# Performance work log

Hardware: AMD Instinct MI355X
Metric: run time of the kernel (lower is better)

The kernel has to match this reference:

```python
import jax, jax.numpy as jnp
import numpy as np

B, S, IN_F, OUT_F, GROUP = 2, 1024, 4096, 4096, 128
N_GROUPS = IN_F // GROUP  # 32


def setup_inputs() -> dict:
    key = jax.random.key(0)
    k1, k2, k3, k4 = jax.random.split(key, 4)
    x = jax.random.normal(k1, (B, S, IN_F), dtype=jnp.float32)
    # int4-range weights stored in int8, symmetric quant in [-7, 7]
    w_q = jax.random.randint(k2, (OUT_F, N_GROUPS, GROUP), -7, 8, dtype=jnp.int8)
    # per-(group, out_feature) scales, positive
    s_w = jax.random.uniform(k3, (N_GROUPS, OUT_F), dtype=jnp.float32,
                             minval=1e-3, maxval=2e-2)
    bias = jax.random.normal(k4, (OUT_F,), dtype=jnp.float32)
    return {"x": x, "w_q": w_q, "s_w": s_w, "bias": bias}


def reference(x, w_q, s_w, bias):
    # Faithful to QuantLinearW4Grouped.forward:
    #   y_g = einsum('ngk,ogk->ngo', x_f, w_f); y = (y_g * s_w[None]).sum(1) + bias
    # Expressed as a single fused einsum (identical math, no (n,g,o) intermediate).
    prefix = x.shape[:-1]
    orig_dtype = x.dtype
    xg = x.reshape(-1, N_GROUPS, GROUP).astype(jnp.float32)  # (n, g, k)
    w_f = w_q.astype(jnp.float32)                            # (o, g, k)
    y = jnp.einsum('ngk,ogk,go->no', xg, w_f, s_w)           # (n, o)
    y = y + bias.astype(y.dtype)
    return y.reshape(*prefix, OUT_F).astype(orig_dtype)
```

## Files before the change

kernel.cpp:

```cpp
#include <hip/hip_runtime.h>
#include <hip/hip_bf16.h>
#include <stdint.h>

#define M_TOK 2048
#define N_OUT 4096
#define K_IN  4096
#define GROUPSZ 128
#define NGRP  32

typedef signed char i8;
typedef int    intx4  __attribute__((ext_vector_type(4)));
typedef float  floatx4 __attribute__((ext_vector_type(4)));

#define AS1 __attribute__((address_space(1)))
#define AS3 __attribute__((address_space(3)))

#define XQ_BLOCKS (M_TOK)
#define WQ_BLOCKS (N_OUT * K_IN / 16 / 256)

__global__ __launch_bounds__(256) void quant_kernel(
    const float* __restrict__ x, const int* __restrict__ wq,
    i8* __restrict__ xq, i8* __restrict__ wq8, float* __restrict__ sx) {
  __shared__ float red[4];
  int b = blockIdx.x;
  int tid = threadIdx.x;
  if (b < XQ_BLOCKS) {
    const float* xr = x + (size_t)b * K_IN;
    int e0 = tid * 16;
    float4 v0 = *(const float4*)(xr + e0);
    float4 v1 = *(const float4*)(xr + e0 + 4);
    float4 v2 = *(const float4*)(xr + e0 + 8);
    float4 v3 = *(const float4*)(xr + e0 + 12);
    float m = fabsf(v0.x);
    m = fmaxf(m, fabsf(v0.y)); m = fmaxf(m, fabsf(v0.z)); m = fmaxf(m, fabsf(v0.w));
    m = fmaxf(m, fabsf(v1.x)); m = fmaxf(m, fabsf(v1.y)); m = fmaxf(m, fabsf(v1.z)); m = fmaxf(m, fabsf(v1.w));
    m = fmaxf(m, fabsf(v2.x)); m = fmaxf(m, fabsf(v2.y)); m = fmaxf(m, fabsf(v2.z)); m = fmaxf(m, fabsf(v2.w));
    m = fmaxf(m, fabsf(v3.x)); m = fmaxf(m, fabsf(v3.y)); m = fmaxf(m, fabsf(v3.z)); m = fmaxf(m, fabsf(v3.w));
#pragma unroll
    for (int off = 32; off > 0; off >>= 1)
      m = fmaxf(m, __shfl_xor(m, off, 64));
    int lane = tid & 63, wv = tid >> 6;
    if (lane == 0) red[wv] = m;
    __syncthreads();
    m = fmaxf(fmaxf(red[0], red[1]), fmaxf(red[2], red[3]));
    float inv = (m > 0.f) ? 127.f / m : 0.f;
    union { i8 q[16]; int4 v; } u;
    u.q[0]  = (i8)(int)rintf(v0.x * inv); u.q[1]  = (i8)(int)rintf(v0.y * inv);
    u.q[2]  = (i8)(int)rintf(v0.z * inv); u.q[3]  = (i8)(int)rintf(v0.w * inv);
    u.q[4]  = (i8)(int)rintf(v1.x * inv); u.q[5]  = (i8)(int)rintf(v1.y * inv);
    u.q[6]  = (i8)(int)rintf(v1.z * inv); u.q[7]  = (i8)(int)rintf(v1.w * inv);
    u.q[8]  = (i8)(int)rintf(v2.x * inv); u.q[9]  = (i8)(int)rintf(v2.y * inv);
    u.q[10] = (i8)(int)rintf(v2.z * inv); u.q[11] = (i8)(int)rintf(v2.w * inv);
    u.q[12] = (i8)(int)rintf(v3.x * inv); u.q[13] = (i8)(int)rintf(v3.y * inv);
    u.q[14] = (i8)(int)rintf(v3.z * inv); u.q[15] = (i8)(int)rintf(v3.w * inv);
    *(int4*)(xq + (size_t)b * K_IN + e0) = u.v;
    if (tid == 0) sx[b] = m * (1.f / 127.f);
  } else {
    size_t t = (size_t)(b - XQ_BLOCKS) * 256 + tid;
    size_t base = t * 16;
    const int* src = wq + base;
    int4 a0 = *(const int4*)(src);
    int4 a1 = *(const int4*)(src + 4);
    int4 a2 = *(const int4*)(src + 8);
    int4 a3 = *(const int4*)(src + 12);
    union { i8 q[16]; int4 v; } u;
    u.q[0]  = (i8)a0.x; u.q[1]  = (i8)a0.y; u.q[2]  = (i8)a0.z; u.q[3]  = (i8)a0.w;
    u.q[4]  = (i8)a1.x; u.q[5]  = (i8)a1.y; u.q[6]  = (i8)a1.z; u.q[7]  = (i8)a1.w;
    u.q[8]  = (i8)a2.x; u.q[9]  = (i8)a2.y; u.q[10] = (i8)a2.z; u.q[11] = (i8)a2.w;
    u.q[12] = (i8)a3.x; u.q[13] = (i8)a3.y; u.q[14] = (i8)a3.z; u.q[15] = (i8)a3.w;
    *(int4*)(wq8 + base) = u.v;
  }
}

#define BM 256
#define BN 128
#define BK 128
#define NT (K_IN / BK)

__global__ __launch_bounds__(512, 2) void gemm_i8_kernel(
    const i8* __restrict__ Aq, const i8* __restrict__ Bq,
    const float* __restrict__ sx, const float* __restrict__ sw,
    const float* __restrict__ bias, float* __restrict__ C) {
  __shared__ i8 As[2 * BM * BK];
  __shared__ i8 Bs[2 * BN * BK];
  __shared__ float sws[NGRP * BN];

  const int tid  = threadIdx.x;
  const int lane = tid & 63;
  const int wave = tid >> 6;
  const int quad = lane >> 4;
  const int l16  = lane & 15;
  const int bm = blockIdx.y;
  const int bn = blockIdx.x;
  const int wm = wave >> 1;
  const int wn = wave & 1;

  const int rowA0 = bm * BM;
  const int rowB0 = bn * BN;

  const i8* srcA[4]; const i8* srcB[2];
#pragma unroll
  for (int i = 0; i < 4; ++i) {
    int chunk = i * 512 + tid;
    int row = chunk >> 3;
    int csw = (chunk & 7) ^ (row & 7);
    srcA[i] = Aq + (size_t)(rowA0 + row) * K_IN + (csw << 4);
  }
#pragma unroll
  for (int i = 0; i < 2; ++i) {
    int chunk = i * 512 + tid;
    int row = chunk >> 3;
    int csw = (chunk & 7) ^ (row & 7);
    srcB[i] = Bq + (size_t)(rowB0 + row) * K_IN + (csw << 4);
  }
  i8* dstA[4]; i8* dstB[2];
#pragma unroll
  for (int i = 0; i < 4; ++i) dstA[i] = As + (size_t)(i * 512 + wave * 64) * 16;
#pragma unroll
  for (int i = 0; i < 2; ++i) dstB[i] = Bs + (size_t)(i * 512 + wave * 64) * 16;

  auto stage = [&](int buf, int t) {
    const size_t ko = (size_t)t * BK;
#pragma unroll
    for (int i = 0; i < 4; ++i)
      __builtin_amdgcn_global_load_lds(
          (const AS1 void*)(srcA[i] + ko),
          (AS3 void*)(dstA[i] + (size_t)buf * (BM * BK)), 16, 0, 0);
#pragma unroll
    for (int i = 0; i < 2; ++i)
      __builtin_amdgcn_global_load_lds(
          (const AS1 void*)(srcB[i] + ko),
          (AS3 void*)(dstB[i] + (size_t)buf * (BN * BK)), 16, 0, 0);
  };

  stage(0, 0);
  {
    int g = tid >> 4, c0 = (tid & 15) * 8;
    const float* src = sw + (size_t)g * N_OUT + rowB0 + c0;
    float* dst = sws + g * BN + c0;
    *(float4*)(dst)     = *(const float4*)(src);
    *(float4*)(dst + 4) = *(const float4*)(src + 4);
  }
  __syncthreads();

  floatx4 master[4][4];
#pragma unroll
  for (int i = 0; i < 4; ++i)
#pragma unroll
    for (int j = 0; j < 4; ++j) master[i][j] = (floatx4)0.0f;

  const intx4 MAGICV = {0x4B400000, 0x4B400000, 0x4B400000, 0x4B400000};
  const float MAGICF = 12582912.0f;

  const int h  = l16 & 7;
  const int x0 = (quad ^ h) << 4;
  const int x1 = x0 ^ 64;

  for (int t = 0; t < NT; ++t) {
    const int cur = t & 1;
    if (t + 1 < NT) {
      stage(cur ^ 1, t + 1);
      asm volatile("s_waitcnt vmcnt(6)" ::: "memory");
    } else {
      asm volatile("s_waitcnt vmcnt(0)" ::: "memory");
    }
    __builtin_amdgcn_s_barrier();

    const i8* Ab = As + (size_t)cur * (BM * BK);
    const i8* Bb = Bs + (size_t)cur * (BN * BK);
    intx4 a[4][2], b[4][2];
#pragma unroll
    for (int i = 0; i < 4; ++i) {
      const i8* pa = Ab + (size_t)(wm * 64 + i * 16 + l16) * BK;
      a[i][0] = *(const intx4*)(pa + x0);
      a[i][1] = *(const intx4*)(pa + x1);
    }
#pragma unroll
    for (int j = 0; j < 4; ++j) {
      const i8* pb = Bb + (size_t)(wn * 64 + j * 16 + l16) * BK;
      b[j][0] = *(const intx4*)(pb + x0);
      b[j][1] = *(const intx4*)(pb + x1);
    }

    float swv[4];
#pragma unroll
    for (int j = 0; j < 4; ++j)
      swv[j] = sws[t * BN + wn * 64 + j * 16 + l16];

    asm volatile("s_waitcnt lgkmcnt(0)" ::: "memory");
    __builtin_amdgcn_s_barrier();

#pragma unroll
    for (int i = 0; i < 4; ++i)
#pragma unroll
      for (int j = 0; j < 4; ++j) {
        intx4 acc = __builtin_amdgcn_mfma_i32_16x16x64_i8(a[i][0], b[j][0], MAGICV, 0, 0, 0);
        acc = __builtin_amdgcn_mfma_i32_16x16x64_i8(a[i][1], b[j][1], acc, 0, 0, 0);
        master[i][j] += (__builtin_bit_cast(floatx4, acc) - MAGICF) * swv[j];
      }
  }

#pragma unroll
  for (int i = 0; i < 4; ++i) {
    float4 sxv = *(const float4*)(sx + rowA0 + wm * 64 + i * 16 + quad * 4);
#pragma unroll
    for (int j = 0; j < 4; ++j) {
      int col = rowB0 + wn * 64 + j * 16 + l16;
      float bv = bias[col];
      int rloc = wm * 64 + i * 16 + quad * 4;
      C[(size_t)(rowA0 + rloc + 0) * N_OUT + col] = master[i][j][0] * sxv.x + bv;
      C[(size_t)(rowA0 + rloc + 1) * N_OUT + col] = master[i][j][1] * sxv.y + bv;
      C[(size_t)(rowA0 + rloc + 2) * N_OUT + col] = master[i][j][2] * sxv.z + bv;
      C[(size_t)(rowA0 + rloc + 3) * N_OUT + col] = master[i][j][3] * sxv.w + bv;
    }
  }
}

extern "C" void kernel_launch(void* const* d_in, const int* in_sizes, int n_in,
                              void* d_out, int out_size, void* d_ws, size_t ws_size,
                              hipStream_t stream) {
  const float* x    = (const float*)d_in[0];
  const int*   wq   = (const int*)d_in[1];
  const float* sw   = (const float*)d_in[2];
  const float* bias = (const float*)d_in[3];
  float* out = (float*)d_out;

  i8*    xq  = (i8*)d_ws;
  i8*    wq8 = (i8*)((char*)d_ws + (size_t)M_TOK * K_IN);
  float* sx  = (float*)((char*)d_ws + (size_t)M_TOK * K_IN
                                     + (size_t)N_OUT * K_IN);

  {
    int nblocks = XQ_BLOCKS + WQ_BLOCKS;
    quant_kernel<<<nblocks, 256, 0, stream>>>(x, wq, xq, wq8, sx);
  }
  {
    dim3 grid(N_OUT / BN, M_TOK / BM);
    gemm_i8_kernel<<<grid, 512, 0, stream>>>(xq, wq8, sx, sw, bias, out);
  }
}
```

Before: 184.1 us.

## Swap GEMM tile to 128x256 and interleave staged loads with split MFMA phases

The block tile changes from 256x128 to 128x256, so each block reuses one A tile across more output columns. The single double-buffered K loop becomes four phases. Each phase issues part of the next tile's global→LDS loads (the B halves, and A two iterations ahead), reads a K-half of fragments, and runs a batch of MFMAs under raised wave priority. The goal is to overlap memory traffic and LDS reads with matrix work instead of stalling at one wait per iteration. In exchange there are many more barriers per iteration and fragile vmcnt bookkeeping.

```diff
diff --git a/kernel.cpp b/kernel.cpp
--- a/kernel.cpp
+++ b/kernel.cpp
@@ -72,8 +72,8 @@
   }
 }
 
-#define BM 256
-#define BN 128
+#define BM 128
+#define BN 256
 #define BK 128
 #define NT (K_IN / BK)
 
@@ -92,54 +92,66 @@
   const int l16  = lane & 15;
   const int bm = blockIdx.y;
   const int bn = blockIdx.x;
-  const int wm = wave >> 1;
-  const int wn = wave & 1;
+  const int wm = wave >> 2;
+  const int wn = wave & 3;
 
   const int rowA0 = bm * BM;
   const int rowB0 = bn * BN;
 
-  const i8* srcA[4]; const i8* srcB[2];
+  const i8* srcA[2]; const i8* srcB[4];
+#pragma unroll
+  for (int i = 0; i < 2; ++i) {
+    int chunk = i * 512 + tid;
+    int row = chunk >> 3;
+    int csw = (chunk & 7) ^ (row & 7);
+    srcA[i] = Aq + (size_t)(rowA0 + row) * K_IN + (csw << 4);
+  }
 #pragma unroll
   for (int i = 0; i < 4; ++i) {
     int chunk = i * 512 + tid;
     int row = chunk >> 3;
     int csw = (chunk & 7) ^ (row & 7);
-    srcA[i] = Aq + (size_t)(rowA0 + row) * K_IN + (csw << 4);
-  }
-#pragma unroll
-  for (int i = 0; i < 2; ++i) {
-    int chunk = i * 512 + tid;
-    int row = chunk >> 3;
-    int csw = (chunk & 7) ^ (row & 7);
     srcB[i] = Bq + (size_t)(rowB0 + row) * K_IN + (csw << 4);
   }
-  i8* dstA[4]; i8* dstB[2];
-#pragma unroll
-  for (int i = 0; i < 4; ++i) dstA[i] = As + (size_t)(i * 512 + wave * 64) * 16;
-#pragma unroll
-  for (int i = 0; i < 2; ++i) dstB[i] = Bs + (size_t)(i * 512 + wave * 64) * 16;
-
-  auto stage = [&](int buf, int t) {
+
+  auto stageA = [&](int buf, int t) {
     const size_t ko = (size_t)t * BK;
 #pragma unroll
-    for (int i = 0; i < 4; ++i)
+    for (int i = 0; i < 2; ++i)
       __builtin_amdgcn_global_load_lds(
           (const AS1 void*)(srcA[i] + ko),
-          (AS3 void*)(dstA[i] + (size_t)buf * (BM * BK)), 16, 0, 0);
+          (AS3 void*)(As + (size_t)buf * (BM * BK) + (size_t)(i * 512 + wave * 64) * 16),
+          16, 0, 0);
+  };
+  auto stageB1 = [&](int buf, int t) {
+    const size_t ko = (size_t)t * BK;
 #pragma unroll
     for (int i = 0; i < 2; ++i)
       __builtin_amdgcn_global_load_lds(
           (const AS1 void*)(srcB[i] + ko),
-          (AS3 void*)(dstB[i] + (size_t)buf * (BN * BK)), 16, 0, 0);
+          (AS3 void*)(Bs + (size_t)buf * (BN * BK) + (size_t)(i * 512 + wave * 64) * 16),
+          16, 0, 0);
   };
-
-  stage(0, 0);
+  auto stageB2 = [&](int buf, int t) {
+    const size_t ko = (size_t)t * BK;
+#pragma unroll
+    for (int i = 2; i < 4; ++i)
+      __builtin_amdgcn_global_load_lds(
+          (const AS1 void*)(srcB[i] + ko),
+          (AS3 void*)(Bs + (size_t)buf * (BN * BK) + (size_t)(i * 512 + wave * 64) * 16),
+          16, 0, 0);
+  };
+
+  stageA(0, 0); stageB1(0, 0); stageB2(0, 0);
+  stageA(1, 1);
   {
-    int g = tid >> 4, c0 = (tid & 15) * 8;
+    int g = tid >> 4, c0 = (tid & 15) * 16;
     const float* src = sw + (size_t)g * N_OUT + rowB0 + c0;
     float* dst = sws + g * BN + c0;
-    *(float4*)(dst)     = *(const float4*)(src);
-    *(float4*)(dst + 4) = *(const float4*)(src + 4);
+    *(float4*)(dst)      = *(const float4*)(src);
+    *(float4*)(dst + 4)  = *(const float4*)(src + 4);
+    *(float4*)(dst + 8)  = *(const float4*)(src + 8);
+    *(float4*)(dst + 12) = *(const float4*)(src + 12);
   }
   __syncthreads();
 
@@ -158,46 +170,91 @@
 
   for (int t = 0; t < NT; ++t) {
     const int cur = t & 1;
-    if (t + 1 < NT) {
-      stage(cur ^ 1, t + 1);
-      asm volatile("s_waitcnt vmcnt(6)" ::: "memory");
-    } else {
-      asm volatile("s_waitcnt vmcnt(0)" ::: "memory");
-    }
-    __builtin_amdgcn_s_barrier();
-
+    const int nxt = cur ^ 1;
     const i8* Ab = As + (size_t)cur * (BM * BK);
     const i8* Bb = Bs + (size_t)cur * (BN * BK);
-    intx4 a[4][2], b[4][2];
-#pragma unroll
-    for (int i = 0; i < 4; ++i) {
-      const i8* pa = Ab + (size_t)(wm * 64 + i * 16 + l16) * BK;
-      a[i][0] = *(const intx4*)(pa + x0);
-      a[i][1] = *(const intx4*)(pa + x1);
-    }
-#pragma unroll
-    for (int j = 0; j < 4; ++j) {
-      const i8* pb = Bb + (size_t)(wn * 64 + j * 16 + l16) * BK;
-      b[j][0] = *(const intx4*)(pb + x0);
-      b[j][1] = *(const intx4*)(pb + x1);
-    }
-
+
+    intx4 a0[4], a1[4], b01[2][2], b23[2][2];
+    intx4 acc01[4][2], acc23[4][2];
     float swv[4];
+
+#pragma unroll
+    for (int i = 0; i < 4; ++i)
+      a0[i] = *(const intx4*)(Ab + (size_t)(wm * 64 + i * 16 + l16) * BK + x0);
+    b01[0][0] = *(const intx4*)(Bb + (size_t)(wn * 64 +  0 + l16) * BK + x0);
+    b01[1][0] = *(const intx4*)(Bb + (size_t)(wn * 64 + 16 + l16) * BK + x0);
 #pragma unroll
     for (int j = 0; j < 4; ++j)
       swv[j] = sws[t * BN + wn * 64 + j * 16 + l16];
-
-    asm volatile("s_waitcnt lgkmcnt(0)" ::: "memory");
-    __builtin_amdgcn_s_barrier();
-
-#pragma unroll
-    for (int i = 0; i < 4; ++i)
-#pragma unroll
-      for (int j = 0; j < 4; ++j) {
-        intx4 acc = __builtin_amdgcn_mfma_i32_16x16x64_i8(a[i][0], b[j][0], MAGICV, 0, 0, 0);
-        acc = __builtin_amdgcn_mfma_i32_16x16x64_i8(a[i][1], b[j][1], acc, 0, 0, 0);
-        master[i][j] += (__builtin_bit_cast(floatx4, acc) - MAGICF) * swv[j];
-      }
+    if (t + 1 < NT) stageB1(nxt, t + 1);
+    __builtin_amdgcn_s_barrier();
+    asm volatile("s_waitcnt lgkmcnt(0)" ::: "memory");
+    __builtin_amdgcn_s_setprio(1);
+#pragma unroll
+    for (int i = 0; i < 4; ++i)
+#pragma unroll
+      for (int j = 0; j < 2; ++j)
+        acc01[i][j] = __builtin_amdgcn_mfma_i32_16x16x64_i8(a0[i], b01[j][0], MAGICV, 0, 0, 0);
+    __builtin_amdgcn_s_setprio(0);
+    __builtin_amdgcn_s_barrier();
+
+#pragma unroll
+    for (int i = 0; i < 4; ++i)
+      a1[i] = *(const intx4*)(Ab + (size_t)(wm * 64 + i * 16 + l16) * BK + x1);
+    b01[0][1] = *(const intx4*)(Bb + (size_t)(wn * 64 +  0 + l16) * BK + x1);
+    b01[1][1] = *(const intx4*)(Bb + (size_t)(wn * 64 + 16 + l16) * BK + x1);
+    if (t + 1 < NT) stageB2(nxt, t + 1);
+    __builtin_amdgcn_s_barrier();
+    asm volatile("s_waitcnt lgkmcnt(0)" ::: "memory");
+    __builtin_amdgcn_s_setprio(1);
+#pragma unroll
+    for (int i = 0; i < 4; ++i)
+#pragma unroll
+      for (int j = 0; j < 2; ++j)
+        acc01[i][j] = __builtin_amdgcn_mfma_i32_16x16x64_i8(a1[i], b01[j][1], acc01[i][j], 0, 0, 0);
+    __builtin_amdgcn_s_setprio(0);
+#pragma unroll
+    for (int i = 0; i < 4; ++i)
+#pragma unroll
+      for (int j = 0; j < 2; ++j)
+        master[i][j] += (__builtin_bit_cast(floatx4, acc01[i][j]) - MAGICF) * swv[j];
+    __builtin_amdgcn_s_barrier();
+
+    b23[0][0] = *(const intx4*)(Bb + (size_t)(wn * 64 + 32 + l16) * BK + x0);
+    b23[1][0] = *(const intx4*)(Bb + (size_t)(wn * 64 + 48 + l16) * BK + x0);
+    if (t + 2 < NT) stageA(cur, t + 2);
+    __builtin_amdgcn_s_barrier();
+    asm volatile("s_waitcnt lgkmcnt(0)" ::: "memory");
+    __builtin_amdgcn_s_setprio(1);
+#pragma unroll
+    for (int i = 0; i < 4; ++i)
+#pragma unroll
+      for (int j = 0; j < 2; ++j)
+        acc23[i][j] = __builtin_amdgcn_mfma_i32_16x16x64_i8(a0[i], b23[j][0], MAGICV, 0, 0, 0);
+    __builtin_amdgcn_s_setprio(0);
+    __builtin_amdgcn_s_barrier();
+
+    b23[0][1] = *(const intx4*)(Bb + (size_t)(wn * 64 + 32 + l16) * BK + x1);
+    b23[1][1] = *(const intx4*)(Bb + (size_t)(wn * 64 + 48 + l16) * BK + x1);
+    if (t + 1 < NT) {
+      if (t + 2 < NT) { asm volatile("s_waitcnt vmcnt(2)" ::: "memory"); }
+      else            { asm volatile("s_waitcnt vmcnt(0)" ::: "memory"); }
+    }
+    __builtin_amdgcn_s_barrier();
+    asm volatile("s_waitcnt lgkmcnt(0)" ::: "memory");
+    __builtin_amdgcn_s_setprio(1);
+#pragma unroll
+    for (int i = 0; i < 4; ++i)
+#pragma unroll
+      for (int j = 0; j < 2; ++j)
+        acc23[i][j] = __builtin_amdgcn_mfma_i32_16x16x64_i8(a1[i], b23[j][1], acc23[i][j], 0, 0, 0);
+    __builtin_amdgcn_s_setprio(0);
+#pragma unroll
+    for (int i = 0; i < 4; ++i)
+#pragma unroll
+      for (int j = 0; j < 2; ++j)
+        master[i][j + 2] += (__builtin_bit_cast(floatx4, acc23[i][j]) - MAGICF) * swv[j + 2];
+    __builtin_amdgcn_s_barrier();
   }
 
 #pragma unroll
```

New measurement: 184.8 us. Within noise of the previous version (+0.4%).
